# Kernel optimization log

Hardware: AMD Instinct MI355X
Metric: run time of the kernel (lower is better)

## Reference

```python
import jax, jax.numpy as jnp
import numpy as np

B, C, N, K, OUT = 4, 192, 10000, 16, 384

def setup_inputs() -> dict:
    key = jax.random.key(0)
    k1, k2, k3, k4 = jax.random.split(key, 4)
    x = jax.random.normal(k1, (B, C, N, 1), dtype=jnp.float32)
    edge_index = jax.random.randint(k2, (2, B, N, K), 0, N, dtype=jnp.int32)
    # 1x1x1 Conv3d weight [OUT, 2C, 1, 1, 1] collapsed to [OUT, 2C]
    fan_in = 2 * C
    weight = jax.random.normal(k3, (OUT, 2 * C), dtype=jnp.float32) / np.sqrt(fan_in)
    bias = jax.random.normal(k4, (OUT,), dtype=jnp.float32) * 0.01
    return {"x": x, "edge_index": edge_index, "weight": weight, "bias": bias}


def _gather_neighbors(x3, idx):
    # x3: [B, C, N], idx: [B, N, K] -> [B, C, N, K]
    return jax.vmap(lambda xb, ib: xb[:, ib])(x3, idx)


def reference(x, edge_index, weight, bias):
    b, c, n, _ = x.shape
    x3 = x[..., 0]                                   # [B, C, N]
    x_i = _gather_neighbors(x3, edge_index[1])       # centers  [B, C, N, K]
    x_j = _gather_neighbors(x3, edge_index[0])       # neighbors [B, C, N, K]
    x_j_max = jnp.max(x_j - x_i, axis=-1)            # max-relative, [B, C, N]
    # torch.cat([x.unsqueeze(2), x_j.unsqueeze(2)], 2).reshape(b, 2c, n, 1)
    # interleaves channels as (x_c, xj_c) pairs
    feat = jnp.stack([x3, x_j_max], axis=2).reshape(b, 2 * c, n)  # [B, 2C, N]
    out = jnp.einsum('oc,bcn->bon', weight, feat) + bias[None, :, None]
    out = jax.nn.relu(out)
    # Conv3d path: output shape [B, OUT, N, 1, 1]
    return out[..., None, None]
```

## Files before the change

### kernel.cpp

```cpp
#include <hip/hip_runtime.h>
#include <hip/hip_bf16.h>


#define NB   4
#define NC   192
#define NN   10000
#define NK   16
#define NOUT 384
#define K2C  384
#define NPAD 10112

typedef short bf16x8 __attribute__((ext_vector_type(8)));
typedef float f32x4  __attribute__((ext_vector_type(4)));

__device__ inline unsigned short f2bf(float f) {
    unsigned int u = __builtin_bit_cast(unsigned int, f);
    u += ((u >> 16) & 1u) + 0x7FFFu;
    return (unsigned short)(u >> 16);
}
__device__ inline float bflo(unsigned int u) {
    return __builtin_bit_cast(float, u << 16);
}
__device__ inline float bfhi(unsigned int u) {
    return __builtin_bit_cast(float, u & 0xFFFF0000u);
}

__global__ __launch_bounds__(256) void k_transpose(const float* __restrict__ x,
                                                   unsigned short* __restrict__ xT) {
    __shared__ unsigned short tile[NC * 65];
    int b  = blockIdx.x & 3;
    int nb = (blockIdx.x >> 2) * 64;
    int t  = threadIdx.x;
    const float* xb = x + (size_t)b * NC * NN;
    for (int i = 0; i < 48; ++i) {
        int idx = i * 256 + t;
        int c  = idx >> 6;
        int nl = idx & 63;
        int n  = nb + nl;
        float v = (n < NN) ? xb[(size_t)c * NN + n] : 0.f;
        tile[c * 65 + nl] = f2bf(v);
    }
    __syncthreads();
    unsigned short* xTb = xT + (size_t)b * NN * NC;
    for (int i = 0; i < 48; ++i) {
        int idx = i * 256 + t;
        int nl  = idx / NC;
        int c   = idx - nl * NC;
        int n   = nb + nl;
        if (n < NN) xTb[(size_t)n * NC + c] = tile[c * 65 + nl];
    }
}

__global__ __launch_bounds__(256) void k_wconv(const float* __restrict__ w,
                                               unsigned short* __restrict__ wbf) {
    int i = blockIdx.x * 256 + threadIdx.x;
    wbf[i] = f2bf(w[i]);
}

__global__ __launch_bounds__(256, 6) void k_gather(const unsigned short* __restrict__ xT,
                                                   const int* __restrict__ eidx,
                                                   unsigned short* __restrict__ featT) {
    int b    = blockIdx.x & 3;
    int tile = blockIdx.x >> 2;
    int wv   = threadIdx.x >> 6;
    int lane = threadIdx.x & 63;
    int lam  = lane & 31;
    int hb   = lane & 32;
    const unsigned int* xr = (const unsigned int*)(xT + (size_t)b * NN * NC);
    unsigned short* fb = featT + (size_t)b * NPAD * K2C;
    int part = lam >> 4;
    const int* ep = eidx + (size_t)part * NB * NN * NK + (size_t)b * NN * NK;

    int nbase = tile * 64 + wv * 16 + (hb ? 8 : 0);

    int v[8];
#pragma unroll
    for (int it = 0; it < 8; ++it) {
        int n = nbase + it;
        v[it] = (n < NN) ? ep[(size_t)n * NK + (lam & 15)] : 0;
    }

    for (int it = 0; it < 8; ++it) {
        int n = nbase + it;
        if (n >= NN) break;
        const unsigned int* crow = xr + (size_t)n * 96;
        unsigned int c0 = crow[lam], c1 = crow[32 + lam], c2 = crow[64 + lam];
        float m0l = -INFINITY, m0h = -INFINITY;
        float m1l = -INFINITY, m1h = -INFINITY;
        float m2l = -INFINITY, m2h = -INFINITY;
#pragma unroll 4
        for (int k = 0; k < 16; ++k) {
            int j = __shfl(v[it], hb + k, 64);
            int i = __shfl(v[it], hb + 16 + k, 64);
            const unsigned int* rj = xr + (size_t)j * 96;
            const unsigned int* ri = xr + (size_t)i * 96;
            unsigned int j0 = rj[lam], j1 = rj[32 + lam], j2 = rj[64 + lam];
            unsigned int i0 = ri[lam], i1 = ri[32 + lam], i2 = ri[64 + lam];
            m0l = fmaxf(m0l, bflo(j0) - bflo(i0));  m0h = fmaxf(m0h, bfhi(j0) - bfhi(i0));
            m1l = fmaxf(m1l, bflo(j1) - bflo(i1));  m1h = fmaxf(m1h, bfhi(j1) - bfhi(i1));
            m2l = fmaxf(m2l, bflo(j2) - bflo(i2));  m2h = fmaxf(m2h, bfhi(j2) - bfhi(i2));
        }
        uint2* orow = (uint2*)(fb + (size_t)n * K2C);
        uint2 o0, o1, o2;
        o0.x = (c0 & 0xFFFFu)  | ((unsigned int)f2bf(m0l) << 16);
        o0.y = (c0 >> 16)      | ((unsigned int)f2bf(m0h) << 16);
        o1.x = (c1 & 0xFFFFu)  | ((unsigned int)f2bf(m1l) << 16);
        o1.y = (c1 >> 16)      | ((unsigned int)f2bf(m1h) << 16);
        o2.x = (c2 & 0xFFFFu)  | ((unsigned int)f2bf(m2l) << 16);
        o2.y = (c2 >> 16)      | ((unsigned int)f2bf(m2h) << 16);
        orow[lam]      = o0;
        orow[32 + lam] = o1;
        orow[64 + lam] = o2;
    }
}

__global__ __launch_bounds__(256, 3) void k_gemm(const unsigned short* __restrict__ wbf,
                                                 const unsigned short* __restrict__ featT,
                                                 const float* __restrict__ bias,
                                                 float* __restrict__ out) {
    __shared__ unsigned short lds[64 * 48 * 8];
    int bid  = blockIdx.x;
    int b    = bid & 3;
    int nt   = bid >> 2;
    int wv   = threadIdx.x >> 6;
    int lane = threadIdx.x & 63;
    int r    = lane & 15;
    int q    = lane >> 4;

    const unsigned short* fbase = featT + (size_t)b * NPAD * K2C + (size_t)(nt * 64) * K2C;
#pragma unroll
    for (int ii = 0; ii < 12; ++ii) {
        int i = wv * 12 + ii;
        unsigned int g = (unsigned int)(i * 64 + lane);
        unsigned int n = g / 48u;
        unsigned int p = g - n * 48u;
        int j = (int)p - (int)((3u * n) % 48u);
        if (j < 0) j += 48;
        const unsigned short* src = fbase + (size_t)n * K2C + (size_t)j * 8;
        __builtin_amdgcn_global_load_lds(
            (const __attribute__((address_space(1))) unsigned int*)src,
            (__attribute__((address_space(3))) unsigned int*)&lds[(size_t)i * 512],
            16, 0, 0);
    }

    const unsigned short* aptr = wbf + (size_t)(wv * 96 + r) * K2C + q * 8;

    unsigned int nbase[4], u0[4];
#pragma unroll
    for (int ni = 0; ni < 4; ++ni) {
        unsigned int n = ni * 16 + r;
        nbase[ni] = n * 48u;
        u0[ni] = ((unsigned int)q + 3u * n) % 48u;
    }

    f32x4 acc[6][4];
#pragma unroll
    for (int mi = 0; mi < 6; ++mi)
#pragma unroll
        for (int ni = 0; ni < 4; ++ni)
            acc[mi][ni] = (f32x4){0.f, 0.f, 0.f, 0.f};

    __syncthreads();

#pragma unroll 2
    for (int t = 0; t < 12; ++t) {
        bf16x8 a[6], bb[4];
#pragma unroll
        for (int mi = 0; mi < 6; ++mi)
            a[mi] = *(const bf16x8*)(aptr + (size_t)mi * 16 * K2C + t * 32);
#pragma unroll
        for (int ni = 0; ni < 4; ++ni) {
            unsigned int u = u0[ni] + 4u * t;
            if (u >= 48u) u -= 48u;
            bb[ni] = *(const bf16x8*)(lds + (size_t)(nbase[ni] + u) * 8);
        }
#pragma unroll
        for (int mi = 0; mi < 6; ++mi)
#pragma unroll
            for (int ni = 0; ni < 4; ++ni)
                acc[mi][ni] = __builtin_amdgcn_mfma_f32_16x16x32_bf16(a[mi], bb[ni], acc[mi][ni], 0, 0, 0);
    }

    float* ob = out + (size_t)b * NOUT * NN;
#pragma unroll
    for (int mi = 0; mi < 6; ++mi) {
        int obase = wv * 96 + mi * 16 + q * 4;
#pragma unroll
        for (int ni = 0; ni < 4; ++ni) {
            int n = nt * 64 + ni * 16 + r;
            if (n < NN) {
#pragma unroll
                for (int rr = 0; rr < 4; ++rr) {
                    int o = obase + rr;
                    float val = acc[mi][ni][rr] + bias[o];
                    ob[(size_t)o * NN + n] = fmaxf(val, 0.f);
                }
            }
        }
    }
}

extern "C" void kernel_launch(void* const* d_in, const int* in_sizes, int n_in,
                              void* d_out, int out_size, void* d_ws, size_t ws_size,
                              hipStream_t stream) {
    const float* x    = (const float*)d_in[0];
    const int*   eidx = (const int*)d_in[1];
    const float* w    = (const float*)d_in[2];
    const float* bias = (const float*)d_in[3];
    float* out = (float*)d_out;

    unsigned short* xT    = (unsigned short*)d_ws;
    unsigned short* featT = xT + (size_t)NB * NN * NC;
    unsigned short* wbf   = featT + (size_t)NB * NPAD * K2C;

    hipLaunchKernelGGL(k_transpose, dim3(4 * 157), dim3(256), 0, stream, x, xT);
    hipLaunchKernelGGL(k_wconv,     dim3(576),     dim3(256), 0, stream, w, wbf);
    hipLaunchKernelGGL(k_gather,    dim3(4 * 157), dim3(256), 0, stream, xT, eidx, featT);
    hipLaunchKernelGGL(k_gemm,      dim3(4 * 158), dim3(256), 0, stream, wbf, featT, bias, out);
}
```

Before: 178.1 us.

## Fuse neighbor gather-max into GEMM via LDS and merge prep kernels

The gather/max-relative stage now writes its interleaved bf16 feature tile straight into the GEMM's LDS buffer, so the featT intermediate no longer makes a round trip through global memory. The transpose and weight-conversion kernels are merged into one prep kernel, which removes launches. The gather now uses 24 lanes per node with 16-byte loads, leaving 40 of 64 lanes idle, and the GEMM now waits behind the gather inside the same block. Bias is also loaded as float4.

Result: slower. 196.4 us (+10.3%).

```diff
diff --git a/kernel.cpp b/kernel.cpp
--- a/kernel.cpp
+++ b/kernel.cpp
@@ -8,7 +8,6 @@
 #define NK   16
 #define NOUT 384
 #define K2C  384
-#define NPAD 10112
 
 typedef short bf16x8 __attribute__((ext_vector_type(8)));
 typedef float f32x4  __attribute__((ext_vector_type(4)));
@@ -18,16 +17,17 @@
     u += ((u >> 16) & 1u) + 0x7FFFu;
     return (unsigned short)(u >> 16);
 }
-__device__ inline float bflo(unsigned int u) {
-    return __builtin_bit_cast(float, u << 16);
-}
-__device__ inline float bfhi(unsigned int u) {
-    return __builtin_bit_cast(float, u & 0xFFFF0000u);
-}
-
-__global__ __launch_bounds__(256) void k_transpose(const float* __restrict__ x,
-                                                   unsigned short* __restrict__ xT) {
+__device__ inline float bflo(unsigned int u) { return __builtin_bit_cast(float, u << 16); }
+__device__ inline float bfhi(unsigned int u) { return __builtin_bit_cast(float, u & 0xFFFF0000u); }
+
+__global__ __launch_bounds__(256) void k_prep(const float* __restrict__ x,
+                                              const float* __restrict__ w,
+                                              unsigned short* __restrict__ xT,
+                                              unsigned short* __restrict__ wbf) {
     __shared__ unsigned short tile[NC * 65];
+    int gid = blockIdx.x * 256 + threadIdx.x;
+    if (gid < NOUT * K2C) wbf[gid] = f2bf(w[gid]);
+
     int b  = blockIdx.x & 3;
     int nb = (blockIdx.x >> 2) * 64;
     int t  = threadIdx.x;
@@ -41,118 +41,110 @@
         tile[c * 65 + nl] = f2bf(v);
     }
     __syncthreads();
-    unsigned short* xTb = xT + (size_t)b * NN * NC;
-    for (int i = 0; i < 48; ++i) {
+    unsigned int* xTd = (unsigned int*)(xT + (size_t)b * NN * NC);
+    for (int i = 0; i < 24; ++i) {
         int idx = i * 256 + t;
-        int nl  = idx / NC;
-        int c   = idx - nl * NC;
+        int nl  = idx / 96;
+        int cd  = idx - nl * 96;
         int n   = nb + nl;
-        if (n < NN) xTb[(size_t)n * NC + c] = tile[c * 65 + nl];
-    }
-}
-
-__global__ __launch_bounds__(256) void k_wconv(const float* __restrict__ w,
-                                               unsigned short* __restrict__ wbf) {
-    int i = blockIdx.x * 256 + threadIdx.x;
-    wbf[i] = f2bf(w[i]);
-}
-
-__global__ __launch_bounds__(256, 6) void k_gather(const unsigned short* __restrict__ xT,
-                                                   const int* __restrict__ eidx,
-                                                   unsigned short* __restrict__ featT) {
-    int b    = blockIdx.x & 3;
-    int tile = blockIdx.x >> 2;
-    int wv   = threadIdx.x >> 6;
-    int lane = threadIdx.x & 63;
-    int lam  = lane & 31;
-    int hb   = lane & 32;
-    const unsigned int* xr = (const unsigned int*)(xT + (size_t)b * NN * NC);
-    unsigned short* fb = featT + (size_t)b * NPAD * K2C;
-    int part = lam >> 4;
-    const int* ep = eidx + (size_t)part * NB * NN * NK + (size_t)b * NN * NK;
-
-    int nbase = tile * 64 + wv * 16 + (hb ? 8 : 0);
-
-    int v[8];
-#pragma unroll
-    for (int it = 0; it < 8; ++it) {
-        int n = nbase + it;
-        v[it] = (n < NN) ? ep[(size_t)n * NK + (lam & 15)] : 0;
-    }
-
-    for (int it = 0; it < 8; ++it) {
-        int n = nbase + it;
-        if (n >= NN) break;
-        const unsigned int* crow = xr + (size_t)n * 96;
-        unsigned int c0 = crow[lam], c1 = crow[32 + lam], c2 = crow[64 + lam];
-        float m0l = -INFINITY, m0h = -INFINITY;
-        float m1l = -INFINITY, m1h = -INFINITY;
-        float m2l = -INFINITY, m2h = -INFINITY;
-#pragma unroll 4
-        for (int k = 0; k < 16; ++k) {
-            int j = __shfl(v[it], hb + k, 64);
-            int i = __shfl(v[it], hb + 16 + k, 64);
-            const unsigned int* rj = xr + (size_t)j * 96;
-            const unsigned int* ri = xr + (size_t)i * 96;
-            unsigned int j0 = rj[lam], j1 = rj[32 + lam], j2 = rj[64 + lam];
-            unsigned int i0 = ri[lam], i1 = ri[32 + lam], i2 = ri[64 + lam];
-            m0l = fmaxf(m0l, bflo(j0) - bflo(i0));  m0h = fmaxf(m0h, bfhi(j0) - bfhi(i0));
-            m1l = fmaxf(m1l, bflo(j1) - bflo(i1));  m1h = fmaxf(m1h, bfhi(j1) - bfhi(i1));
-            m2l = fmaxf(m2l, bflo(j2) - bflo(i2));  m2h = fmaxf(m2h, bfhi(j2) - bfhi(i2));
-        }
-        uint2* orow = (uint2*)(fb + (size_t)n * K2C);
-        uint2 o0, o1, o2;
-        o0.x = (c0 & 0xFFFFu)  | ((unsigned int)f2bf(m0l) << 16);
-        o0.y = (c0 >> 16)      | ((unsigned int)f2bf(m0h) << 16);
-        o1.x = (c1 & 0xFFFFu)  | ((unsigned int)f2bf(m1l) << 16);
-        o1.y = (c1 >> 16)      | ((unsigned int)f2bf(m1h) << 16);
-        o2.x = (c2 & 0xFFFFu)  | ((unsigned int)f2bf(m2l) << 16);
-        o2.y = (c2 >> 16)      | ((unsigned int)f2bf(m2h) << 16);
-        orow[lam]      = o0;
-        orow[32 + lam] = o1;
-        orow[64 + lam] = o2;
-    }
-}
-
-__global__ __launch_bounds__(256, 3) void k_gemm(const unsigned short* __restrict__ wbf,
-                                                 const unsigned short* __restrict__ featT,
-                                                 const float* __restrict__ bias,
-                                                 float* __restrict__ out) {
+        if (n < NN) {
+            unsigned int lo = tile[(2 * cd)     * 65 + nl];
+            unsigned int hi = tile[(2 * cd + 1) * 65 + nl];
+            xTd[(size_t)n * 96 + cd] = lo | (hi << 16);
+        }
+    }
+}
+
+__global__ __launch_bounds__(256, 3) void k_fused(const unsigned short* __restrict__ wbf,
+                                                  const unsigned short* __restrict__ xT,
+                                                  const int* __restrict__ eidx,
+                                                  const float* __restrict__ bias,
+                                                  float* __restrict__ out) {
     __shared__ unsigned short lds[64 * 48 * 8];
     int bid  = blockIdx.x;
     int b    = bid & 3;
     int nt   = bid >> 2;
     int wv   = threadIdx.x >> 6;
     int lane = threadIdx.x & 63;
-    int r    = lane & 15;
-    int q    = lane >> 4;
-
-    const unsigned short* fbase = featT + (size_t)b * NPAD * K2C + (size_t)(nt * 64) * K2C;
-#pragma unroll
-    for (int ii = 0; ii < 12; ++ii) {
-        int i = wv * 12 + ii;
-        unsigned int g = (unsigned int)(i * 64 + lane);
-        unsigned int n = g / 48u;
-        unsigned int p = g - n * 48u;
-        int j = (int)p - (int)((3u * n) % 48u);
-        if (j < 0) j += 48;
-        const unsigned short* src = fbase + (size_t)n * K2C + (size_t)j * 8;
-        __builtin_amdgcn_global_load_lds(
-            (const __attribute__((address_space(1))) unsigned int*)src,
-            (__attribute__((address_space(3))) unsigned int*)&lds[(size_t)i * 512],
-            16, 0, 0);
-    }
-
+
+    const uint4* xr4 = (const uint4*)(xT + (size_t)b * NN * NC);
+    const int* e0 = eidx + (size_t)b * NN * NK;
+    const int* e1 = eidx + (size_t)NB * NN * NK + (size_t)b * NN * NK;
+    int nbase = nt * 64 + wv * 16;
+
+    int vj[4], vi[4];
+#pragma unroll
+    for (int i = 0; i < 4; ++i) {
+        int idx = i * 64 + lane;
+        int n   = nbase + (idx >> 4);
+        vj[i] = (n < NN) ? e0[(size_t)nbase * NK + idx] : 0;
+        vi[i] = (n < NN) ? e1[(size_t)nbase * NK + idx] : 0;
+    }
+    int d = lane;
+    bool act = (d < 24);
+
+#pragma unroll
+    for (int qq = 0; qq < 4; ++qq) {
+        int vjq = vj[qq], viq = vi[qq];
+        for (int it2 = 0; it2 < 4; ++it2) {
+            int it = qq * 4 + it2;
+            int n  = nbase + it;
+            if (n < NN) {
+                int nl = wv * 16 + it;
+                uint4 cx = make_uint4(0, 0, 0, 0);
+                if (act) cx = xr4[(size_t)n * 24 + d];
+                float m[8];
+#pragma unroll
+                for (int c = 0; c < 8; ++c) m[c] = -1e30f;
+#pragma unroll
+                for (int k = 0; k < 16; ++k) {
+                    int sl  = it2 * 16 + k;
+                    int jn  = __shfl(vjq, sl, 64);
+                    int in_ = __shfl(viq, sl, 64);
+                    uint4 jr = make_uint4(0, 0, 0, 0), ir = make_uint4(0, 0, 0, 0);
+                    if (act) { jr = xr4[(size_t)jn * 24 + d]; ir = xr4[(size_t)in_ * 24 + d]; }
+                    m[0] = fmaxf(m[0], bflo(jr.x) - bflo(ir.x));
+                    m[1] = fmaxf(m[1], bfhi(jr.x) - bfhi(ir.x));
+                    m[2] = fmaxf(m[2], bflo(jr.y) - bflo(ir.y));
+                    m[3] = fmaxf(m[3], bfhi(jr.y) - bfhi(ir.y));
+                    m[4] = fmaxf(m[4], bflo(jr.z) - bflo(ir.z));
+                    m[5] = fmaxf(m[5], bfhi(jr.z) - bfhi(ir.z));
+                    m[6] = fmaxf(m[6], bflo(jr.w) - bflo(ir.w));
+                    m[7] = fmaxf(m[7], bfhi(jr.w) - bfhi(ir.w));
+                }
+                if (act) {
+                    unsigned int mm[4];
+#pragma unroll
+                    for (int c = 0; c < 4; ++c)
+                        mm[c] = (unsigned int)f2bf(m[2 * c]) | ((unsigned int)f2bf(m[2 * c + 1]) << 16);
+                    uint4 g0, g1;
+                    g0.x = (cx.x & 0xFFFFu) | (mm[0] << 16);
+                    g0.y = (cx.x >> 16)     | (mm[0] & 0xFFFF0000u);
+                    g0.z = (cx.y & 0xFFFFu) | (mm[1] << 16);
+                    g0.w = (cx.y >> 16)     | (mm[1] & 0xFFFF0000u);
+                    g1.x = (cx.z & 0xFFFFu) | (mm[2] << 16);
+                    g1.y = (cx.z >> 16)     | (mm[2] & 0xFFFF0000u);
+                    g1.z = (cx.w & 0xFFFFu) | (mm[3] << 16);
+                    g1.w = (cx.w >> 16)     | (mm[3] & 0xFFFF0000u);
+                    int s0 = nl * 48 + (2 * d     + 3 * nl) % 48;
+                    int s1 = nl * 48 + (2 * d + 1 + 3 * nl) % 48;
+                    *(uint4*)&lds[(size_t)s0 * 8] = g0;
+                    *(uint4*)&lds[(size_t)s1 * 8] = g1;
+                }
+            }
+        }
+    }
+
+    int r = lane & 15;
+    int q = lane >> 4;
     const unsigned short* aptr = wbf + (size_t)(wv * 96 + r) * K2C + q * 8;
-
-    unsigned int nbase[4], u0[4];
+    unsigned int nbs[4], u0[4];
 #pragma unroll
     for (int ni = 0; ni < 4; ++ni) {
-        unsigned int n = ni * 16 + r;
-        nbase[ni] = n * 48u;
-        u0[ni] = ((unsigned int)q + 3u * n) % 48u;
-    }
-
+        unsigned int n_ = ni * 16 + r;
+        nbs[ni] = n_ * 48u;
+        u0[ni]  = ((unsigned int)q + 3u * n_) % 48u;
+    }
     f32x4 acc[6][4];
 #pragma unroll
     for (int mi = 0; mi < 6; ++mi)
@@ -172,7 +164,7 @@
         for (int ni = 0; ni < 4; ++ni) {
             unsigned int u = u0[ni] + 4u * t;
             if (u >= 48u) u -= 48u;
-            bb[ni] = *(const bf16x8*)(lds + (size_t)(nbase[ni] + u) * 8);
+            bb[ni] = *(const bf16x8*)(lds + (size_t)(nbs[ni] + u) * 8);
         }
 #pragma unroll
         for (int mi = 0; mi < 6; ++mi)
@@ -185,15 +177,16 @@
 #pragma unroll
     for (int mi = 0; mi < 6; ++mi) {
         int obase = wv * 96 + mi * 16 + q * 4;
+        float4 b4 = *(const float4*)(bias + obase);
 #pragma unroll
         for (int ni = 0; ni < 4; ++ni) {
             int n = nt * 64 + ni * 16 + r;
             if (n < NN) {
+                float bv[4] = {b4.x, b4.y, b4.z, b4.w};
 #pragma unroll
                 for (int rr = 0; rr < 4; ++rr) {
-                    int o = obase + rr;
-                    float val = acc[mi][ni][rr] + bias[o];
-                    ob[(size_t)o * NN + n] = fmaxf(val, 0.f);
+                    float val = acc[mi][ni][rr] + bv[rr];
+                    ob[(size_t)(obase + rr) * NN + n] = fmaxf(val, 0.f);
                 }
             }
         }
@@ -209,12 +202,9 @@
     const float* bias = (const float*)d_in[3];
     float* out = (float*)d_out;
 
-    unsigned short* xT    = (unsigned short*)d_ws;
-    unsigned short* featT = xT + (size_t)NB * NN * NC;
-    unsigned short* wbf   = featT + (size_t)NB * NPAD * K2C;
-
-    hipLaunchKernelGGL(k_transpose, dim3(4 * 157), dim3(256), 0, stream, x, xT);
-    hipLaunchKernelGGL(k_wconv,     dim3(576),     dim3(256), 0, stream, w, wbf);
-    hipLaunchKernelGGL(k_gather,    dim3(4 * 157), dim3(256), 0, stream, xT, eidx, featT);
-    hipLaunchKernelGGL(k_gemm,      dim3(4 * 158), dim3(256), 0, stream, wbf, featT, bias, out);
-}
+    unsigned short* xT  = (unsigned short*)d_ws;
+    unsigned short* wbf = xT + (size_t)NB * NN * NC;
+
+    hipLaunchKernelGGL(k_prep,  dim3(4 * 157), dim3(256), 0, stream, x, w, xT, wbf);
+    hipLaunchKernelGGL(k_fused, dim3(4 * 157), dim3(256), 0, stream, wbf, xT, eidx, bias, out);
+}
```
